# Optimization experiments

Hardware: AMD Instinct MI355X
Metric: run time of the kernel (lower is better)

Reference implementation:

```python
import jax, jax.numpy as jnp
import numpy as np

N = 100_000      # nodes
M = 200_000      # hyperedges
E = 1_000_000    # incidence pairs
D_IN = 64
HEADS, D_OUT = 8, 16   # linear out = 8*16 = 128


def setup_inputs() -> dict:
    key = jax.random.key(0)
    k = jax.random.split(key, 7)
    X = jax.random.normal(k[0], (N, D_IN), dtype=jnp.float32)
    vertex = jax.random.randint(k[1], (E,), 0, N, dtype=jnp.int32)
    edges = jax.random.randint(k[2], (E,), 0, M, dtype=jnp.int32)
    dege = jax.random.uniform(k[3], (M, 1), dtype=jnp.float32)
    degv = jax.random.uniform(k[4], (N, 1), dtype=jnp.float32)
    W = jax.random.normal(k[5], (D_IN, HEADS * D_OUT), dtype=jnp.float32) / np.sqrt(D_IN)
    b = jax.random.normal(k[6], (HEADS * D_OUT,), dtype=jnp.float32) * 0.01
    return {"X": X, "vertex": vertex, "edges": edges, "dege": dege, "degv": degv, "W": W, "b": b}


def reference(X, vertex, edges, dege, degv, W, b):
    n_nodes = X.shape[0]
    n_edges = dege.shape[0]
    # vertex -> hyperedge aggregation (first_aggregate = 'mean')
    Xve = X[vertex]                                               # [E, D]
    sums = jax.ops.segment_sum(Xve, edges, num_segments=n_edges)  # [M, D]
    counts = jax.ops.segment_sum(jnp.ones((edges.shape[0],), X.dtype), edges, num_segments=n_edges)
    Xe = sums / jnp.maximum(counts, 1.0)[:, None]                 # empty edges -> 0
    Xe = Xe * dege
    # hyperedge -> vertex aggregation (sum)
    Xev = Xe[edges]                                               # [E, D]
    Xv = jax.ops.segment_sum(Xev, vertex, num_segments=n_nodes)   # [N, D]
    Xv = Xv * degv
    # normalize_l2: row norm is computed on a DETACHED tensor in torch
    rownorm = jnp.linalg.norm(jax.lax.stop_gradient(Xv), axis=1, keepdims=True)
    scale = jnp.where(rownorm > 0, 1.0 / rownorm, 0.0)
    Xn = Xv * scale
    return Xn @ W + b
```

## Files before the change

### kernel.cpp

```cpp
#include <hip/hip_runtime.h>


#define DIN 64
#define DOUT 128
#define CH 4096
#define BSHIFT 9
#define FINE 512
#define PAYBITS 18
#define PAYMASK ((1u << PAYBITS) - 1u)
#define XB 256

typedef float f32x4 __attribute__((ext_vector_type(4)));
typedef short bf16x8 __attribute__((ext_vector_type(8)));

__device__ __forceinline__ unsigned short f2b(float f) {
  unsigned u = __float_as_uint(f);
  u = u + 0x7fffu + ((u >> 16) & 1u);
  return (unsigned short)(u >> 16);
}
__device__ __forceinline__ float b2f(unsigned s) {
  return __uint_as_float(s << 16);
}

__global__ __launch_bounds__(256) void k_p1(
    const int* __restrict__ vertex, const int* __restrict__ edges,
    int* __restrict__ G, const float* __restrict__ X,
    unsigned short* __restrict__ Xb, int* __restrict__ done,
    int E, int BKE, int BK, int NCH, int total4) {
  if (blockIdx.x == 0 && threadIdx.x == 0) *done = 0;
  if (blockIdx.x >= (unsigned)NCH) {
    int xb = blockIdx.x - NCH;
    for (int i = xb * 256 + threadIdx.x; i < total4; i += XB * 256) {
      float4 a = ((const float4*)X)[i];
      ushort4 r;
      r.x = f2b(a.x); r.y = f2b(a.y); r.z = f2b(a.z); r.w = f2b(a.w);
      ((ushort4*)Xb)[i] = r;
    }
    return;
  }
  __shared__ int h[1024];
  for (int i = threadIdx.x; i < BK; i += 256) h[i] = 0;
  __syncthreads();
  int c = blockIdx.x;
  int s = c * CH, e_ = min(E, s + CH);
  int n4 = (e_ - s) >> 2;
  const int4* ep = (const int4*)(edges + s);
  const int4* vp = (const int4*)(vertex + s);
  for (int i = threadIdx.x; i < n4; i += 256) {
    int4 ee = ep[i], vv = vp[i];
    atomicAdd(&h[ee.x >> BSHIFT], 1); atomicAdd(&h[ee.y >> BSHIFT], 1);
    atomicAdd(&h[ee.z >> BSHIFT], 1); atomicAdd(&h[ee.w >> BSHIFT], 1);
    atomicAdd(&h[BKE + (vv.x >> BSHIFT)], 1); atomicAdd(&h[BKE + (vv.y >> BSHIFT)], 1);
    atomicAdd(&h[BKE + (vv.z >> BSHIFT)], 1); atomicAdd(&h[BKE + (vv.w >> BSHIFT)], 1);
  }
  for (int i = s + (n4 << 2) + threadIdx.x; i < e_; i += 256) {
    atomicAdd(&h[edges[i] >> BSHIFT], 1);
    atomicAdd(&h[BKE + (vertex[i] >> BSHIFT)], 1);
  }
  __syncthreads();
  for (int b = threadIdx.x; b < BK; b += 256) G[(size_t)b * NCH + c] = h[b];
}

__global__ __launch_bounds__(256) void k_p1b(
    int* __restrict__ G, int* __restrict__ rowTot, int* __restrict__ bucketBase,
    int* __restrict__ done, int NCH, int BK) {
  int b = blockIdx.x;
  int* row = G + (size_t)b * NCH;
  __shared__ int wsum[4];
  __shared__ int carry;
  __shared__ bool amLast;
  if (threadIdx.x == 0) carry = 0;
  __syncthreads();
  for (int base = 0; base < NCH; base += 256) {
    int i = base + threadIdx.x;
    int v = (i < NCH) ? row[i] : 0;
    int lane = threadIdx.x & 63, wid = threadIdx.x >> 6;
    int inc = v;
    #pragma unroll
    for (int o = 1; o < 64; o <<= 1) {
      int t = __shfl_up(inc, o);
      if (lane >= o) inc += t;
    }
    if (lane == 63) wsum[wid] = inc;
    __syncthreads();
    int woff = carry;
    for (int w = 0; w < wid; ++w) woff += wsum[w];
    int excl = woff + inc - v;
    if (i < NCH) row[i] = excl;
    __syncthreads();
    if (threadIdx.x == 0) carry += wsum[0] + wsum[1] + wsum[2] + wsum[3];
    __syncthreads();
  }
  if (threadIdx.x == 0) {
    rowTot[b] = carry;
    __threadfence();
    amLast = (atomicAdd(done, 1) == gridDim.x - 1);
  }
  __syncthreads();
  if (!amLast) return;

  if (threadIdx.x == 0) carry = 0;
  __syncthreads();
  for (int base = 0; base < BK; base += 256) {
    int i = base + threadIdx.x;
    int v = (i < BK) ? atomicAdd(&rowTot[i], 0) : 0;
    int lane = threadIdx.x & 63, wid = threadIdx.x >> 6;
    int inc = v;
    #pragma unroll
    for (int o = 1; o < 64; o <<= 1) {
      int t = __shfl_up(inc, o);
      if (lane >= o) inc += t;
    }
    if (lane == 63) wsum[wid] = inc;
    __syncthreads();
    int woff = carry;
    for (int w = 0; w < wid; ++w) woff += wsum[w];
    int excl = woff + inc - v;
    if (i < BK) bucketBase[i] = excl;
    __syncthreads();
    if (threadIdx.x == 0) carry += wsum[0] + wsum[1] + wsum[2] + wsum[3];
    __syncthreads();
  }
  if (threadIdx.x == 0) bucketBase[BK] = carry;
}

__global__ __launch_bounds__(256) void p2_scatter(
    const int* __restrict__ vertex, const int* __restrict__ edges,
    const int* __restrict__ G, const int* __restrict__ bucketBase,
    unsigned* __restrict__ temp, int E, int BKE, int BK, int NCH) {
  __shared__ int curs[1024];
  int c = blockIdx.x;
  for (int b = threadIdx.x; b < BK; b += 256)
    curs[b] = bucketBase[b] + G[(size_t)b * NCH + c];
  __syncthreads();
  int s = c * CH, e_ = min(E, s + CH);
  for (int i = s + threadIdx.x; i < e_; i += 256) {
    int e = edges[i], v = vertex[i];
    int pE = atomicAdd(&curs[e >> BSHIFT], 1);
    temp[pE] = ((unsigned)(e & (FINE - 1)) << PAYBITS) | (unsigned)v;
    int pV = atomicAdd(&curs[BKE + (v >> BSHIFT)], 1);
    temp[pV] = ((unsigned)(v & (FINE - 1)) << PAYBITS) | (unsigned)e;
  }
}

__global__ __launch_bounds__(256) void p3_sort(
    const unsigned* __restrict__ temp, const int* __restrict__ bucketBase,
    int* __restrict__ off, int* __restrict__ perm, int BKE, int M, int N) {
  __shared__ int hist[FINE];
  __shared__ int pos[FINE];
  __shared__ int wsum[4];
  int g = blockIdx.x;
  bool isE = g < BKE;
  int gg = isE ? g : g - BKE;
  int keyBase = gg << BSHIFT;
  int cap = isE ? M : N;
  int offBase = (isE ? 0 : M) + keyBase;
  int fineCount = min(FINE, cap - keyBase);
  int pairBase = bucketBase[g], pairEnd = bucketBase[g + 1];
  int cnt = pairEnd - pairBase;

  for (int i = threadIdx.x; i < FINE; i += 256) hist[i] = 0;
  __syncthreads();
  for (int i = threadIdx.x; i < cnt; i += 256)
    atomicAdd(&hist[temp[pairBase + i] >> PAYBITS], 1);
  __syncthreads();

  int t2 = threadIdx.x * 2;
  int a0 = hist[t2], a1 = hist[t2 + 1];
  int tsum = a0 + a1;
  int lane = threadIdx.x & 63, wid = threadIdx.x >> 6;
  int inc = tsum;
  #pragma unroll
  for (int o = 1; o < 64; o <<= 1) {
    int t = __shfl_up(inc, o);
    if (lane >= o) inc += t;
  }
  if (lane == 63) wsum[wid] = inc;
  __syncthreads();
  int woff = 0;
  for (int w = 0; w < wid; ++w) woff += wsum[w];
  int excl = woff + inc - tsum;
  pos[t2] = excl; pos[t2 + 1] = excl + a0;
  __syncthreads();

  for (int f = threadIdx.x; f < fineCount; f += 256)
    off[offBase + f] = pairBase + pos[f] + hist[f];
  for (int f = threadIdx.x; f < FINE; f += 256) pos[f] += pairBase;
  __syncthreads();

  for (int i = threadIdx.x; i < cnt; i += 256) {
    unsigned p = temp[pairBase + i];
    int q = atomicAdd(&pos[p >> PAYBITS], 1);
    perm[q] = (int)(p & PAYMASK);
  }
}


__global__ __launch_bounds__(256) void k_edge(
    const unsigned short* __restrict__ Xb, const int* __restrict__ off,
    const int* __restrict__ perm, const float* __restrict__ dege,
    unsigned short* __restrict__ Xe, int M) {
  long long gid = (long long)blockIdx.x * 256 + threadIdx.x;
  int wv = (int)(gid >> 6);
  int lane = threadIdx.x & 63;
  int g = lane >> 3, li = lane & 7;
  int e = wv * 8 + g;
  bool valid = e < M;
  int start = 0, end = 0;
  if (valid) { start = e ? off[e - 1] : 0; end = off[e]; }
  int deg = end - start;
  int myidx = (valid && li < deg) ? perm[start + li] : 0;
  int jmax = min(deg, 8);
  int jw = jmax;
  jw = max(jw, __shfl_xor(jw, 8));
  jw = max(jw, __shfl_xor(jw, 16));
  jw = max(jw, __shfl_xor(jw, 32));
  const uint4* X4 = (const uint4*)Xb;
  float acc[8] = {0.f, 0.f, 0.f, 0.f, 0.f, 0.f, 0.f, 0.f};
  #pragma unroll 4
  for (int j = 0; j < jw; ++j) {
    int v0 = __shfl(myidx, (g << 3) + j);
    if (j < jmax) {
      uint4 a = X4[(size_t)v0 * 8 + li];
      acc[0] += b2f(a.x & 0xffffu); acc[1] += b2f(a.x >> 16);
      acc[2] += b2f(a.y & 0xffffu); acc[3] += b2f(a.y >> 16);
      acc[4] += b2f(a.z & 0xffffu); acc[5] += b2f(a.z >> 16);
      acc[6] += b2f(a.w & 0xffffu); acc[7] += b2f(a.w >> 16);
    }
  }
  for (int j = 8; j < deg; ++j) {
    int v0 = perm[start + j];
    uint4 a = X4[(size_t)v0 * 8 + li];
    acc[0] += b2f(a.x & 0xffffu); acc[1] += b2f(a.x >> 16);
    acc[2] += b2f(a.y & 0xffffu); acc[3] += b2f(a.y >> 16);
    acc[4] += b2f(a.z & 0xffffu); acc[5] += b2f(a.z >> 16);
    acc[6] += b2f(a.w & 0xffffu); acc[7] += b2f(a.w >> 16);
  }
  if (valid) {
    float s = dege[e] / fmaxf((float)deg, 1.0f);
    uint4 r;
    r.x = (unsigned)f2b(acc[0] * s) | ((unsigned)f2b(acc[1] * s) << 16);
    r.y = (unsigned)f2b(acc[2] * s) | ((unsigned)f2b(acc[3] * s) << 16);
    r.z = (unsigned)f2b(acc[4] * s) | ((unsigned)f2b(acc[5] * s) << 16);
    r.w = (unsigned)f2b(acc[6] * s) | ((unsigned)f2b(acc[7] * s) << 16);
    ((uint4*)Xe)[(size_t)e * 8 + li] = r;
  }
}

__global__ __launch_bounds__(256) void k_nodeagg(
    const unsigned short* __restrict__ Xe, const int* __restrict__ off,
    const int* __restrict__ perm, const float* __restrict__ degv,
    unsigned short* __restrict__ xn, int N, int M) {
  long long gid = (long long)blockIdx.x * 256 + threadIdx.x;
  int wv = (int)(gid >> 6);
  int lane = threadIdx.x & 63;
  int g = lane >> 4, li = lane & 15;
  int base = wv * 8;
  int nA = base + g;
  int nB = base + 4 + g;
  bool vA = nA < N, vB = nB < N;
  int sA = 0, eA = 0, sB = 0, eB = 0;
  if (vA) { sA = off[M + nA - 1]; eA = off[M + nA]; }
  if (vB) { sB = off[M + nB - 1]; eB = off[M + nB]; }
  int dA = eA - sA, dB = eB - sB;
  int myA = (vA && li < dA) ? perm[sA + li] : 0;
  int myB = (vB && li < dB) ? perm[sB + li] : 0;
  int jA = min(dA, 16), jB = min(dB, 16);
  int jw = max(jA, jB);
  jw = max(jw, __shfl_xor(jw, 16));
  jw = max(jw, __shfl_xor(jw, 32));
  const uint2* Xe2 = (const uint2*)Xe;
  float4 aA = make_float4(0.f, 0.f, 0.f, 0.f);
  float4 aB = make_float4(0.f, 0.f, 0.f, 0.f);
  #pragma unroll 2
  for (int j = 0; j < jw; ++j) {
    int iA = __shfl(myA, (g << 4) + j);
    int iB = __shfl(myB, (g << 4) + j);
    if (j < jA) {
      uint2 a = Xe2[(size_t)iA * 16 + li];
      aA.x += b2f(a.x & 0xffffu); aA.y += b2f(a.x >> 16);
      aA.z += b2f(a.y & 0xffffu); aA.w += b2f(a.y >> 16);
    }
    if (j < jB) {
      uint2 a = Xe2[(size_t)iB * 16 + li];
      aB.x += b2f(a.x & 0xffffu); aB.y += b2f(a.x >> 16);
      aB.z += b2f(a.y & 0xffffu); aB.w += b2f(a.y >> 16);
    }
  }
  for (int j = 16; j < dA; ++j) {
    int e0 = perm[sA + j];
    uint2 a = Xe2[(size_t)e0 * 16 + li];
    aA.x += b2f(a.x & 0xffffu); aA.y += b2f(a.x >> 16);
    aA.z += b2f(a.y & 0xffffu); aA.w += b2f(a.y >> 16);
  }
  for (int j = 16; j < dB; ++j) {
    int e0 = perm[sB + j];
    uint2 a = Xe2[(size_t)e0 * 16 + li];
    aB.x += b2f(a.x & 0xffffu); aB.y += b2f(a.x >> 16);
    aB.z += b2f(a.y & 0xffffu); aB.w += b2f(a.y >> 16);
  }
  float dvA = vA ? degv[nA] : 0.f;
  float dvB = vB ? degv[nB] : 0.f;
  aA.x *= dvA; aA.y *= dvA; aA.z *= dvA; aA.w *= dvA;
  aB.x *= dvB; aB.y *= dvB; aB.z *= dvB; aB.w *= dvB;
  float ssA = aA.x * aA.x + aA.y * aA.y + aA.z * aA.z + aA.w * aA.w;
  float ssB = aB.x * aB.x + aB.y * aB.y + aB.z * aB.z + aB.w * aB.w;
  #pragma unroll
  for (int o = 1; o <= 8; o <<= 1) {
    ssA += __shfl_xor(ssA, o);
    ssB += __shfl_xor(ssB, o);
  }
  float scA = ssA > 0.0f ? 1.0f / sqrtf(ssA) : 0.0f;
  float scB = ssB > 0.0f ? 1.0f / sqrtf(ssB) : 0.0f;
  if (vA) {
    ushort4 r;
    r.x = f2b(aA.x * scA); r.y = f2b(aA.y * scA);
    r.z = f2b(aA.z * scA); r.w = f2b(aA.w * scA);
    ((ushort4*)xn)[(size_t)nA * 16 + li] = r;
  }
  if (vB) {
    ushort4 r;
    r.x = f2b(aB.x * scB); r.y = f2b(aB.y * scB);
    r.z = f2b(aB.z * scB); r.w = f2b(aB.w * scB);
    ((ushort4*)xn)[(size_t)nB * 16 + li] = r;
  }
}

#define WPAD 72
__global__ __launch_bounds__(256) void k_linear(
    const unsigned short* __restrict__ xn, const float* __restrict__ W,
    const float* __restrict__ bias, float* __restrict__ out, int N) {
  __shared__ unsigned short Wt[DOUT * WPAD];
  for (int i = threadIdx.x; i < DIN * DOUT; i += 256) {
    int k = i >> 7, c = i & 127;
    Wt[c * WPAD + k] = f2b(W[i]);
  }
  __syncthreads();
  int lane = threadIdx.x & 63;
  int wid = threadIdx.x >> 6;
  int r = lane & 15, h = lane >> 4;

  bf16x8 Bf[8][2];
  #pragma unroll
  for (int c = 0; c < 8; ++c) {
    #pragma unroll
    for (int ks = 0; ks < 2; ++ks) {
      int col = c * 16 + r;
      int k0 = ks * 32 + h * 8;
      Bf[c][ks] = *(const bf16x8*)&Wt[col * WPAD + k0];
    }
  }
  float bcol[8];
  #pragma unroll
  for (int c = 0; c < 8; ++c) bcol[c] = bias[c * 16 + r];

  int strips = (N + 15) >> 4;
  for (int s = blockIdx.x * 4 + wid; s < strips; s += gridDim.x * 4) {
    int row0 = s << 4;
    const unsigned short* xrow = xn + (size_t)(row0 + r) * DIN;
    bf16x8 a0 = *(const bf16x8*)&xrow[h * 8];
    bf16x8 a1 = *(const bf16x8*)&xrow[32 + h * 8];
    #pragma unroll
    for (int c = 0; c < 8; ++c) {
      f32x4 acc = {bcol[c], bcol[c], bcol[c], bcol[c]};
      acc = __builtin_amdgcn_mfma_f32_16x16x32_bf16(a0, Bf[c][0], acc, 0, 0, 0);
      acc = __builtin_amdgcn_mfma_f32_16x16x32_bf16(a1, Bf[c][1], acc, 0, 0, 0);
      #pragma unroll
      for (int q = 0; q < 4; ++q)
        out[(size_t)(row0 + h * 4 + q) * DOUT + c * 16 + r] = acc[q];
    }
  }
}

extern "C" void kernel_launch(void* const* d_in, const int* in_sizes, int n_in,
                              void* d_out, int out_size, void* d_ws, size_t ws_size,
                              hipStream_t stream) {
  const float* X      = (const float*)d_in[0];
  const int*   vertex = (const int*)d_in[1];
  const int*   edges  = (const int*)d_in[2];
  const float* dege   = (const float*)d_in[3];
  const float* degv   = (const float*)d_in[4];
  const float* W      = (const float*)d_in[5];
  const float* b      = (const float*)d_in[6];
  float* out = (float*)d_out;

  int N = in_sizes[0] / DIN;
  int E = in_sizes[1];
  int M = in_sizes[3];

  int NCH = (E + CH - 1) / CH;
  int BKE = (M + FINE - 1) >> BSHIFT;
  int BKV = (N + FINE - 1) >> BSHIFT;
  int BK  = BKE + BKV;

  unsigned short* Xe = (unsigned short*)d_ws;
  unsigned short* Xb = Xe + (size_t)M * DIN;
  int*   off  = (int*)(Xb + (size_t)N * DIN);
  int*   perm = off + (M + N);
  char*  R    = (char*)(perm + 2 * (size_t)E);
  unsigned*       temp = (unsigned*)R;
  unsigned short* xn   = (unsigned short*)R;
  size_t rBytes = (size_t)2 * E * 4;
  size_t xBytes = (size_t)N * DIN * 2;
  char*  R2   = R + (rBytes > xBytes ? rBytes : xBytes);
  int*   G    = (int*)R2;
  int*   rowTot = G + (size_t)BK * NCH;
  int*   bucketBase = rowTot + BK;
  int*   done = bucketBase + BK + 1;

  int total4 = N * DIN / 4;
  k_p1<<<NCH + XB, 256, 0, stream>>>(vertex, edges, G, X, Xb, done,
                                     E, BKE, BK, NCH, total4);
  k_p1b<<<BK, 256, 0, stream>>>(G, rowTot, bucketBase, done, NCH, BK);
  p2_scatter<<<NCH, 256, 0, stream>>>(vertex, edges, G, bucketBase, temp,
                                      E, BKE, BK, NCH);
  p3_sort<<<BK, 256, 0, stream>>>(temp, bucketBase, off, perm, BKE, M, N);

  int edgeBlocks = (M + 31) / 32;
  k_edge<<<edgeBlocks, 256, 0, stream>>>(Xb, off, perm, dege, Xe, M);

  int nodeWaves = (N + 7) / 8;
  int nodeBlocks = (nodeWaves + 3) / 4;
  k_nodeagg<<<nodeBlocks, 256, 0, stream>>>(Xe, off, perm, degv, xn, N, M);

  int strips = (N + 15) >> 4;
  int linBlocks = (strips + 3) / 4;
  k_linear<<<linBlocks, 256, 0, stream>>>(xn, W, b, out, N);
}
```

Baseline: 135.7 us.

## Vectorize scatter loads, stage bucket pairs in LDS, widen node-gather loads

The scatter kernel now reads edges and vertex as int4 and processes four incidences per iteration. The bucket sort kernel copies a bucket's pairs into a 32KB shared buffer on the first pass and reads them back from there, so temp is read from global memory only once. The node aggregation kernel switches from 16 lanes with 8-byte loads to 8 lanes with 16-byte loads per node, each node's neighbour list split into two chunks of eight. The 32KB of extra LDS may reduce occupancy in the sort kernel, and the int4 loads assume the chunk start is 16-byte aligned.

```diff
diff --git a/kernel.cpp b/kernel.cpp
--- a/kernel.cpp
+++ b/kernel.cpp
@@ -9,6 +9,7 @@
 #define PAYBITS 18
 #define PAYMASK ((1u << PAYBITS) - 1u)
 #define XB 256
+#define STAGE 8192
 
 typedef float f32x4 __attribute__((ext_vector_type(4)));
 typedef short bf16x8 __attribute__((ext_vector_type(8)));
@@ -134,7 +135,30 @@
     curs[b] = bucketBase[b] + G[(size_t)b * NCH + c];
   __syncthreads();
   int s = c * CH, e_ = min(E, s + CH);
-  for (int i = s + threadIdx.x; i < e_; i += 256) {
+  int n4 = (e_ - s) >> 2;
+  const int4* ep = (const int4*)(edges + s);
+  const int4* vp = (const int4*)(vertex + s);
+  for (int i = threadIdx.x; i < n4; i += 256) {
+    int4 ee = ep[i], vv = vp[i];
+    int p;
+    p = atomicAdd(&curs[ee.x >> BSHIFT], 1);
+    temp[p] = ((unsigned)(ee.x & (FINE - 1)) << PAYBITS) | (unsigned)vv.x;
+    p = atomicAdd(&curs[BKE + (vv.x >> BSHIFT)], 1);
+    temp[p] = ((unsigned)(vv.x & (FINE - 1)) << PAYBITS) | (unsigned)ee.x;
+    p = atomicAdd(&curs[ee.y >> BSHIFT], 1);
+    temp[p] = ((unsigned)(ee.y & (FINE - 1)) << PAYBITS) | (unsigned)vv.y;
+    p = atomicAdd(&curs[BKE + (vv.y >> BSHIFT)], 1);
+    temp[p] = ((unsigned)(vv.y & (FINE - 1)) << PAYBITS) | (unsigned)ee.y;
+    p = atomicAdd(&curs[ee.z >> BSHIFT], 1);
+    temp[p] = ((unsigned)(ee.z & (FINE - 1)) << PAYBITS) | (unsigned)vv.z;
+    p = atomicAdd(&curs[BKE + (vv.z >> BSHIFT)], 1);
+    temp[p] = ((unsigned)(vv.z & (FINE - 1)) << PAYBITS) | (unsigned)ee.z;
+    p = atomicAdd(&curs[ee.w >> BSHIFT], 1);
+    temp[p] = ((unsigned)(ee.w & (FINE - 1)) << PAYBITS) | (unsigned)vv.w;
+    p = atomicAdd(&curs[BKE + (vv.w >> BSHIFT)], 1);
+    temp[p] = ((unsigned)(vv.w & (FINE - 1)) << PAYBITS) | (unsigned)ee.w;
+  }
+  for (int i = s + (n4 << 2) + threadIdx.x; i < e_; i += 256) {
     int e = edges[i], v = vertex[i];
     int pE = atomicAdd(&curs[e >> BSHIFT], 1);
     temp[pE] = ((unsigned)(e & (FINE - 1)) << PAYBITS) | (unsigned)v;
@@ -149,6 +173,7 @@
   __shared__ int hist[FINE];
   __shared__ int pos[FINE];
   __shared__ int wsum[4];
+  __shared__ unsigned pairsS[STAGE];
   int g = blockIdx.x;
   bool isE = g < BKE;
   int gg = isE ? g : g - BKE;
@@ -158,11 +183,20 @@
   int fineCount = min(FINE, cap - keyBase);
   int pairBase = bucketBase[g], pairEnd = bucketBase[g + 1];
   int cnt = pairEnd - pairBase;
+  bool staged = cnt <= STAGE;
 
   for (int i = threadIdx.x; i < FINE; i += 256) hist[i] = 0;
   __syncthreads();
-  for (int i = threadIdx.x; i < cnt; i += 256)
-    atomicAdd(&hist[temp[pairBase + i] >> PAYBITS], 1);
+  if (staged) {
+    for (int i = threadIdx.x; i < cnt; i += 256) {
+      unsigned p = temp[pairBase + i];
+      pairsS[i] = p;
+      atomicAdd(&hist[p >> PAYBITS], 1);
+    }
+  } else {
+    for (int i = threadIdx.x; i < cnt; i += 256)
+      atomicAdd(&hist[temp[pairBase + i] >> PAYBITS], 1);
+  }
   __syncthreads();
 
   int t2 = threadIdx.x * 2;
@@ -188,10 +222,18 @@
   for (int f = threadIdx.x; f < FINE; f += 256) pos[f] += pairBase;
   __syncthreads();
 
-  for (int i = threadIdx.x; i < cnt; i += 256) {
-    unsigned p = temp[pairBase + i];
-    int q = atomicAdd(&pos[p >> PAYBITS], 1);
-    perm[q] = (int)(p & PAYMASK);
+  if (staged) {
+    for (int i = threadIdx.x; i < cnt; i += 256) {
+      unsigned p = pairsS[i];
+      int q = atomicAdd(&pos[p >> PAYBITS], 1);
+      perm[q] = (int)(p & PAYMASK);
+    }
+  } else {
+    for (int i = threadIdx.x; i < cnt; i += 256) {
+      unsigned p = temp[pairBase + i];
+      int q = atomicAdd(&pos[p >> PAYBITS], 1);
+      perm[q] = (int)(p & PAYMASK);
+    }
   }
 }
 
@@ -254,75 +296,66 @@
   long long gid = (long long)blockIdx.x * 256 + threadIdx.x;
   int wv = (int)(gid >> 6);
   int lane = threadIdx.x & 63;
-  int g = lane >> 4, li = lane & 15;
-  int base = wv * 8;
-  int nA = base + g;
-  int nB = base + 4 + g;
-  bool vA = nA < N, vB = nB < N;
-  int sA = 0, eA = 0, sB = 0, eB = 0;
-  if (vA) { sA = off[M + nA - 1]; eA = off[M + nA]; }
-  if (vB) { sB = off[M + nB - 1]; eB = off[M + nB]; }
-  int dA = eA - sA, dB = eB - sB;
-  int myA = (vA && li < dA) ? perm[sA + li] : 0;
-  int myB = (vB && li < dB) ? perm[sB + li] : 0;
-  int jA = min(dA, 16), jB = min(dB, 16);
-  int jw = max(jA, jB);
-  jw = max(jw, __shfl_xor(jw, 16));
-  jw = max(jw, __shfl_xor(jw, 32));
-  const uint2* Xe2 = (const uint2*)Xe;
-  float4 aA = make_float4(0.f, 0.f, 0.f, 0.f);
-  float4 aB = make_float4(0.f, 0.f, 0.f, 0.f);
-  #pragma unroll 2
-  for (int j = 0; j < jw; ++j) {
-    int iA = __shfl(myA, (g << 4) + j);
-    int iB = __shfl(myB, (g << 4) + j);
-    if (j < jA) {
-      uint2 a = Xe2[(size_t)iA * 16 + li];
-      aA.x += b2f(a.x & 0xffffu); aA.y += b2f(a.x >> 16);
-      aA.z += b2f(a.y & 0xffffu); aA.w += b2f(a.y >> 16);
-    }
-    if (j < jB) {
-      uint2 a = Xe2[(size_t)iB * 16 + li];
-      aB.x += b2f(a.x & 0xffffu); aB.y += b2f(a.x >> 16);
-      aB.z += b2f(a.y & 0xffffu); aB.w += b2f(a.y >> 16);
-    }
-  }
-  for (int j = 16; j < dA; ++j) {
-    int e0 = perm[sA + j];
-    uint2 a = Xe2[(size_t)e0 * 16 + li];
-    aA.x += b2f(a.x & 0xffffu); aA.y += b2f(a.x >> 16);
-    aA.z += b2f(a.y & 0xffffu); aA.w += b2f(a.y >> 16);
-  }
-  for (int j = 16; j < dB; ++j) {
-    int e0 = perm[sB + j];
-    uint2 a = Xe2[(size_t)e0 * 16 + li];
-    aB.x += b2f(a.x & 0xffffu); aB.y += b2f(a.x >> 16);
-    aB.z += b2f(a.y & 0xffffu); aB.w += b2f(a.y >> 16);
-  }
-  float dvA = vA ? degv[nA] : 0.f;
-  float dvB = vB ? degv[nB] : 0.f;
-  aA.x *= dvA; aA.y *= dvA; aA.z *= dvA; aA.w *= dvA;
-  aB.x *= dvB; aB.y *= dvB; aB.z *= dvB; aB.w *= dvB;
-  float ssA = aA.x * aA.x + aA.y * aA.y + aA.z * aA.z + aA.w * aA.w;
-  float ssB = aB.x * aB.x + aB.y * aB.y + aB.z * aB.z + aB.w * aB.w;
+  int g = lane >> 3, li = lane & 7;
+  int node = wv * 8 + g;
+  bool valid = node < N;
+  int start = 0, end = 0;
+  if (valid) { start = off[M + node - 1]; end = off[M + node]; }
+  int deg = end - start;
+  int my0 = (valid && li < deg) ? perm[start + li] : 0;
+  int my1 = (valid && 8 + li < deg) ? perm[start + 8 + li] : 0;
+  int jmax0 = min(deg, 8);
+  int jmax1 = min(max(deg - 8, 0), 8);
+  int jw0 = jmax0, jw1 = jmax1;
+  jw0 = max(jw0, __shfl_xor(jw0, 8)); jw1 = max(jw1, __shfl_xor(jw1, 8));
+  jw0 = max(jw0, __shfl_xor(jw0, 16)); jw1 = max(jw1, __shfl_xor(jw1, 16));
+  jw0 = max(jw0, __shfl_xor(jw0, 32)); jw1 = max(jw1, __shfl_xor(jw1, 32));
+  const uint4* Xe4 = (const uint4*)Xe;
+  float acc[8] = {0.f, 0.f, 0.f, 0.f, 0.f, 0.f, 0.f, 0.f};
+  #pragma unroll 4
+  for (int j = 0; j < jw0; ++j) {
+    int e0 = __shfl(my0, (g << 3) + j);
+    if (j < jmax0) {
+      uint4 a = Xe4[(size_t)e0 * 8 + li];
+      acc[0] += b2f(a.x & 0xffffu); acc[1] += b2f(a.x >> 16);
+      acc[2] += b2f(a.y & 0xffffu); acc[3] += b2f(a.y >> 16);
+      acc[4] += b2f(a.z & 0xffffu); acc[5] += b2f(a.z >> 16);
+      acc[6] += b2f(a.w & 0xffffu); acc[7] += b2f(a.w >> 16);
+    }
+  }
+  #pragma unroll 4
+  for (int j = 0; j < jw1; ++j) {
+    int e0 = __shfl(my1, (g << 3) + j);
+    if (j < jmax1) {
+      uint4 a = Xe4[(size_t)e0 * 8 + li];
+      acc[0] += b2f(a.x & 0xffffu); acc[1] += b2f(a.x >> 16);
+      acc[2] += b2f(a.y & 0xffffu); acc[3] += b2f(a.y >> 16);
+      acc[4] += b2f(a.z & 0xffffu); acc[5] += b2f(a.z >> 16);
+      acc[6] += b2f(a.w & 0xffffu); acc[7] += b2f(a.w >> 16);
+    }
+  }
+  for (int j = 16; j < deg; ++j) {
+    int e0 = perm[start + j];
+    uint4 a = Xe4[(size_t)e0 * 8 + li];
+    acc[0] += b2f(a.x & 0xffffu); acc[1] += b2f(a.x >> 16);
+    acc[2] += b2f(a.y & 0xffffu); acc[3] += b2f(a.y >> 16);
+    acc[4] += b2f(a.z & 0xffffu); acc[5] += b2f(a.z >> 16);
+    acc[6] += b2f(a.w & 0xffffu); acc[7] += b2f(a.w >> 16);
+  }
+  float dv = valid ? degv[node] : 0.f;
+  float ss = 0.f;
   #pragma unroll
-  for (int o = 1; o <= 8; o <<= 1) {
-    ssA += __shfl_xor(ssA, o);
-    ssB += __shfl_xor(ssB, o);
-  }
-  float scA = ssA > 0.0f ? 1.0f / sqrtf(ssA) : 0.0f;
-  float scB = ssB > 0.0f ? 1.0f / sqrtf(ssB) : 0.0f;
-  if (vA) {
-    ushort4 r;
-    r.x = f2b(aA.x * scA); r.y = f2b(aA.y * scA);
-    r.z = f2b(aA.z * scA); r.w = f2b(aA.w * scA);
-    ((ushort4*)xn)[(size_t)nA * 16 + li] = r;
-  }
-  if (vB) {
-    ushort4 r;
-    r.x = f2b(aB.x * scB); r.y = f2b(aB.y * scB);
-    r.z = f2b(aB.z * scB); r.w = f2b(aB.w * scB);
-    ((ushort4*)xn)[(size_t)nB * 16 + li] = r;
+  for (int i = 0; i < 8; ++i) { acc[i] *= dv; ss += acc[i] * acc[i]; }
+  #pragma unroll
+  for (int o = 1; o <= 4; o <<= 1) ss += __shfl_xor(ss, o);
+  float sc = ss > 0.0f ? 1.0f / sqrtf(ss) : 0.0f;
+  if (valid) {
+    uint4 r;
+    r.x = (unsigned)f2b(acc[0] * sc) | ((unsigned)f2b(acc[1] * sc) << 16);
+    r.y = (unsigned)f2b(acc[2] * sc) | ((unsigned)f2b(acc[3] * sc) << 16);
+    r.z = (unsigned)f2b(acc[4] * sc) | ((unsigned)f2b(acc[5] * sc) << 16);
+    r.w = (unsigned)f2b(acc[6] * sc) | ((unsigned)f2b(acc[7] * sc) << 16);
+    ((uint4*)xn)[(size_t)node * 8 + li] = r;
   }
 }
 
```

Result: faster. 131.5 us (-3.1%).
